# Kernel optimization log

Hardware: AMD Instinct MI355X
Metric: run time of the kernel (lower is better)

Reference implementation:

```python
import jax, jax.numpy as jnp
import numpy as np

N_NODES = 100_000
N_EDGES = 1_600_000
N_GRAPHS = 64
NUM_TYPES = 8192
EMBED = 64
HID = 128
N_STEPS = 6
N_ETYPES = 3
OUT = 1


def setup_inputs() -> dict:
    key = jax.random.key(0)
    ks = jax.random.split(key, 20)
    s = 0.05
    return {
        "type_ids": jax.random.randint(ks[0], (N_NODES,), 0, NUM_TYPES),
        "src": jax.random.randint(ks[1], (N_EDGES,), 0, N_NODES),
        "dst": jax.random.randint(ks[2], (N_EDGES,), 0, N_NODES),
        "etypes": jax.random.randint(ks[3], (N_EDGES,), 0, N_ETYPES),
        "graph_ids": jnp.sort(jax.random.randint(ks[4], (N_NODES,), 0, N_GRAPHS)),
        "embed_table": jax.random.normal(ks[5], (NUM_TYPES, EMBED)) * s,
        "W_red": jax.random.normal(ks[6], (HID, EMBED)) * s,
        "b_red": jnp.zeros((HID,)),
        "W_msg": jax.random.normal(ks[7], (N_ETYPES, HID, HID)) * s,
        "b_msg": jnp.zeros((N_ETYPES, HID)),
        "W_ih": jax.random.normal(ks[8], (3 * HID, HID)) * s,
        "b_ih": jnp.zeros((3 * HID,)),
        "W_hh": jax.random.normal(ks[9], (3 * HID, HID)) * s,
        "b_hh": jnp.zeros((3 * HID,)),
        "W_gate": jax.random.normal(ks[10], (1, 2 * HID)) * s,
        "b_gate": jnp.zeros((1,)),
        "W_out": jax.random.normal(ks[11], (OUT, 2 * HID)) * s,
        "b_out": jnp.zeros((OUT,)),
    }


def _gru_cell(x, h, W_ih, b_ih, W_hh, b_hh):
    gi = x @ W_ih.T + b_ih  # [N, 3H]
    gh = h @ W_hh.T + b_hh
    i_r, i_z, i_n = jnp.split(gi, 3, axis=-1)
    h_r, h_z, h_n = jnp.split(gh, 3, axis=-1)
    r = jax.nn.sigmoid(i_r + h_r)
    z = jax.nn.sigmoid(i_z + h_z)
    n = jnp.tanh(i_n + r * h_n)
    return (1.0 - z) * n + z * h


def reference(type_ids, src, dst, etypes, graph_ids, embed_table, W_red, b_red,
              W_msg, b_msg, W_ih, b_ih, W_hh, b_hh, W_gate, b_gate, W_out, b_out):
    ann = embed_table[type_ids]                 # [N, EMBED]
    h0 = ann @ W_red.T + b_red                  # [N, HID]
    h = h0
    edge_idx = etypes * N_NODES + src           # flat index into [K*N, H]
    for _ in range(N_STEPS):
        # per-etype linear applied at node level, then gathered per edge
        trans = jnp.einsum('nh,kdh->knd', h, W_msg) + b_msg[:, None, :]  # [K,N,H]
        msg = trans.reshape(N_ETYPES * N_NODES, HID)[edge_idx]           # [E,H]
        a = jax.ops.segment_sum(msg, dst, num_segments=N_NODES)          # [N,H]
        h = _gru_cell(a, h, W_ih, b_ih, W_hh, b_hh)
    feat = jnp.concatenate([h, h0], axis=-1)    # [N, 2H]
    # global attention pooling: segment softmax over graphs
    gate = feat @ W_gate.T + b_gate             # [N,1]
    m = jax.ops.segment_max(gate, graph_ids, num_segments=N_GRAPHS)
    e = jnp.exp(gate - m[graph_ids])
    ssum = jax.ops.segment_sum(e, graph_ids, num_segments=N_GRAPHS)
    alpha = e / ssum[graph_ids]                 # [N,1]
    readout = jax.ops.segment_sum(alpha * feat, graph_ids, num_segments=N_GRAPHS)
    return readout @ W_out.T + b_out            # [G, OUT]
```

## Files before the change

kernel.cpp:

```cpp
#include <hip/hip_runtime.h>

#define NN 100000
#define NE 1600000
#define NG 64

typedef __attribute__((ext_vector_type(8))) short bf16x8;
typedef __attribute__((ext_vector_type(4))) float f32x4;

__device__ __forceinline__ unsigned short f2bf(float f) {
  unsigned u = __float_as_uint(f);
  unsigned r = u + 0x7FFFu + ((u >> 16) & 1u);
  return (unsigned short)(r >> 16);
}
__device__ __forceinline__ float bf2f(unsigned u16) {
  return __uint_as_float(u16 << 16);
}

__device__ __forceinline__ float wave_sum(float v) {
#pragma unroll
  for (int off = 32; off; off >>= 1) v += __shfl_down(v, off, 64);
  return v;
}
__device__ __forceinline__ float wave_max(float v) {
#pragma unroll
  for (int off = 32; off; off >>= 1) v = fmaxf(v, __shfl_down(v, off, 64));
  return v;
}

__device__ __forceinline__ float sigm(float v) { return 1.f / (1.f + __expf(-v)); }

__global__ void __launch_bounds__(256)
gather_k(const unsigned* __restrict__ hbf32, const int* __restrict__ rowst,
         const int* __restrict__ payload, unsigned short* __restrict__ S) {
  const int lane = threadIdx.x & 63, wid = threadIdx.x >> 6;
  int task = blockIdx.x * 4 + wid;
  if (task >= 3 * NN) return;
  const int s = rowst[task], e = rowst[task + 1];
  float sx = 0.f, sy = 0.f;
  int i = s;
  for (; i + 4 <= e; i += 4) {
    int p0 = payload[i], p1 = payload[i + 1], p2 = payload[i + 2], p3 = payload[i + 3];
    unsigned v0 = hbf32[(size_t)p0 * 64 + lane];
    unsigned v1 = hbf32[(size_t)p1 * 64 + lane];
    unsigned v2 = hbf32[(size_t)p2 * 64 + lane];
    unsigned v3 = hbf32[(size_t)p3 * 64 + lane];
    sx += bf2f(v0 & 0xffffu) + bf2f(v1 & 0xffffu) + bf2f(v2 & 0xffffu) + bf2f(v3 & 0xffffu);
    sy += bf2f(v0 >> 16) + bf2f(v1 >> 16) + bf2f(v2 >> 16) + bf2f(v3 >> 16);
  }
  const int rem = e - i;
  if (rem == 3) {
    int p0 = payload[i], p1 = payload[i + 1], p2 = payload[i + 2];
    unsigned v0 = hbf32[(size_t)p0 * 64 + lane];
    unsigned v1 = hbf32[(size_t)p1 * 64 + lane];
    unsigned v2 = hbf32[(size_t)p2 * 64 + lane];
    sx += bf2f(v0 & 0xffffu) + bf2f(v1 & 0xffffu) + bf2f(v2 & 0xffffu);
    sy += bf2f(v0 >> 16) + bf2f(v1 >> 16) + bf2f(v2 >> 16);
  } else if (rem == 2) {
    int p0 = payload[i], p1 = payload[i + 1];
    unsigned v0 = hbf32[(size_t)p0 * 64 + lane];
    unsigned v1 = hbf32[(size_t)p1 * 64 + lane];
    sx += bf2f(v0 & 0xffffu) + bf2f(v1 & 0xffffu);
    sy += bf2f(v0 >> 16) + bf2f(v1 >> 16);
  } else if (rem == 1) {
    int p0 = payload[i];
    unsigned v0 = hbf32[(size_t)p0 * 64 + lane];
    sx += bf2f(v0 & 0xffffu);
    sy += bf2f(v0 >> 16);
  }
  const int et = task / NN;
  const int n = task - et * NN;
  unsigned pk = (unsigned)f2bf(sx) | ((unsigned)f2bf(sy) << 16);
  *(unsigned*)(S + (size_t)n * 384 + et * 128 + 2 * lane) = pk;
}

__global__ void pack_fragB(const float* __restrict__ W, unsigned short* __restrict__ WF) {
  int idx = blockIdx.x * 256 + threadIdx.x;
  if (idx >= 3 * 4 * 8 * 64) return;
  int lane = idx & 63;
  int cc = (idx >> 6) & 7;
  int ks = (idx >> 9) & 3;
  int g = idx >> 11;
  int col = cc * 16 + (lane & 15);
  int k0 = ks * 32 + (lane >> 4) * 8;
  const float* src = W + ((size_t)g * 128 + col) * 128 + k0;
  bf16x8 o;
#pragma unroll
  for (int j = 0; j < 8; ++j) o[j] = (short)f2bf(src[j]);
  *(bf16x8*)(WF + (size_t)idx * 8) = o;
}

__global__ void pack_rz(const float* __restrict__ Wih, const float* __restrict__ Whh,
                        unsigned short* __restrict__ WF) {
  int idx = blockIdx.x * 256 + threadIdx.x;
  if (idx >= 2 * 8 * 8 * 64) return;
  int lane = idx & 63;
  int cc = (idx >> 6) & 7;
  int ks = (idx >> 9) & 7;
  int g = idx >> 12;
  int col = cc * 16 + (lane & 15);
  int k0 = ks * 32 + (lane >> 4) * 8;
  int row = g * 128 + col;
  const float* src = (k0 < 128) ? (Wih + (size_t)row * 128 + k0)
                                : (Whh + (size_t)row * 128 + (k0 - 128));
  bf16x8 o;
#pragma unroll
  for (int j = 0; j < 8; ++j) o[j] = (short)f2bf(src[j]);
  *(bf16x8*)(WF + (size_t)idx * 8) = o;
}

__global__ void pack_cat384(const float* __restrict__ Wmsg, unsigned short* __restrict__ WF) {
  int idx = blockIdx.x * 256 + threadIdx.x;
  if (idx >= 12 * 8 * 64) return;
  int lane = idx & 63;
  int cc = (idx >> 6) & 7;
  int ks = idx >> 9;
  int col = cc * 16 + (lane & 15);
  int k0 = ks * 32 + (lane >> 4) * 8;
  int et = k0 >> 7, h0 = k0 & 127;
  const float* src = Wmsg + (size_t)et * 16384 + (size_t)col * 128 + h0;
  bf16x8 o;
#pragma unroll
  for (int j = 0; j < 8; ++j) o[j] = (short)f2bf(src[j]);
  *(bf16x8*)(WF + (size_t)idx * 8) = o;
}

__global__ void __launch_bounds__(256, 4)
msg_gemm6(const unsigned short* __restrict__ S, const unsigned short* __restrict__ WcatF,
          const float* __restrict__ bmsg, const int* __restrict__ rowst,
          unsigned short* __restrict__ abf) {
  __shared__ char Ss[24576];
  const int tid = threadIdx.x, lane = tid & 63, wid = tid >> 6;
  const int l15 = lane & 15, lhi = lane >> 4;
  const int bm = blockIdx.x * 32;
  const int wrow0 = (wid >> 1) * 16, wcol0 = (wid & 1) * 64;

  for (int idx = tid; idx < 1536; idx += 256) {
    int row = idx / 48, o = (idx - row * 48) * 16;
    int gr = bm + row;
    uint4 v = make_uint4(0, 0, 0, 0);
    if (gr < NN) v = *(const uint4*)((const char*)S + (size_t)gr * 768 + o);
    *(uint4*)(Ss + row * 768 + (o ^ ((row & 7) << 4))) = v;
  }
  __syncthreads();

  f32x4 acc[4];
#pragma unroll
  for (int f = 0; f < 4; ++f)
#pragma unroll
    for (int r = 0; r < 4; ++r) acc[f][r] = 0.f;

#pragma unroll
  for (int ks = 0; ks < 12; ++ks) {
    int kb = ks * 64 + lhi * 16;
    int row = wrow0 + l15;
    bf16x8 fS = *(const bf16x8*)(Ss + row * 768 + (kb ^ ((row & 7) << 4)));
#pragma unroll
    for (int nf = 0; nf < 4; ++nf) {
      bf16x8 bw = *(const bf16x8*)(WcatF +
          (((size_t)ks * 8 + (wcol0 >> 4) + nf) * 64 + lane) * 8);
      acc[nf] = __builtin_amdgcn_mfma_f32_16x16x32_bf16(fS, bw, acc[nf], 0, 0, 0);
    }
  }

#pragma unroll
  for (int r = 0; r < 4; ++r) {
    int grow = bm + wrow0 + lhi * 4 + r;
    if (grow >= NN) continue;
    float d0 = (float)(rowst[grow + 1] - rowst[grow]);
    float d1 = (float)(rowst[NN + grow + 1] - rowst[NN + grow]);
    float d2 = (float)(rowst[2 * NN + grow + 1] - rowst[2 * NN + grow]);
#pragma unroll
    for (int nf = 0; nf < 4; ++nf) {
      int col = wcol0 + nf * 16 + l15;
      float v = acc[nf][r] + d0 * bmsg[col] + d1 * bmsg[128 + col] +
                d2 * bmsg[256 + col];
      abf[(size_t)grow * 128 + col] = f2bf(v);
    }
  }
}

__global__ void __launch_bounds__(256, 4)
gru6(unsigned short* __restrict__ hbf, unsigned short* __restrict__ hlo,
     const unsigned short* __restrict__ abf, const unsigned short* __restrict__ WrzF,
     const unsigned short* __restrict__ WihF, const unsigned short* __restrict__ WhhF,
     const float* __restrict__ bih, const float* __restrict__ bhh) {
  __shared__ char cat[32 * 512];
  const int tid = threadIdx.x, lane = tid & 63, wid = tid >> 6;
  const int l15 = lane & 15, lhi = lane >> 4;
  const int bm = blockIdx.x * 32;
  const int wrow0 = (wid >> 1) * 16, wcol0 = (wid & 1) * 64;

  for (int idx = tid; idx < 1024; idx += 256) {
    int row = idx >> 5, seg = idx & 31;
    int gr = bm + row;
    uint4 v = make_uint4(0, 0, 0, 0);
    if (gr < NN) {
      if (seg < 16)
        v = *(const uint4*)((const char*)abf + (size_t)gr * 256 + seg * 16);
      else
        v = *(const uint4*)((const char*)hbf + (size_t)gr * 256 + (seg - 16) * 16);
    }
    int o = seg * 16;
    *(uint4*)(cat + row * 512 + (o ^ ((row & 7) << 4))) = v;
  }
  __syncthreads();

  f32x4 rr[4];
  {
    f32x4 acc[4];
#pragma unroll
    for (int f = 0; f < 4; ++f)
#pragma unroll
      for (int r = 0; r < 4; ++r) acc[f][r] = 0.f;
#pragma unroll
    for (int ks = 0; ks < 8; ++ks) {
      int kb = ks * 64 + lhi * 16;
      int row = wrow0 + l15;
      bf16x8 fA = *(const bf16x8*)(cat + row * 512 + (kb ^ ((row & 7) << 4)));
#pragma unroll
      for (int nf = 0; nf < 4; ++nf) {
        bf16x8 bw = *(const bf16x8*)(WrzF +
            (((size_t)ks * 8 + (wcol0 >> 4) + nf) * 64 + lane) * 8);
        acc[nf] = __builtin_amdgcn_mfma_f32_16x16x32_bf16(fA, bw, acc[nf], 0, 0, 0);
      }
    }
#pragma unroll
    for (int f = 0; f < 4; ++f) {
      int col = wcol0 + f * 16 + l15;
      float b = bih[col] + bhh[col];
#pragma unroll
      for (int r = 0; r < 4; ++r) rr[f][r] = sigm(acc[f][r] + b);
    }
  }

  f32x4 nn[4];
  {
    f32x4 acc_i[4], acc_h[4];
#pragma unroll
    for (int f = 0; f < 4; ++f)
#pragma unroll
      for (int r = 0; r < 4; ++r) { acc_i[f][r] = 0.f; acc_h[f][r] = 0.f; }
#pragma unroll
    for (int ks = 0; ks < 4; ++ks) {
      int kb = ks * 64 + lhi * 16;
      int row = wrow0 + l15;
      int sw = (row & 7) << 4;
      bf16x8 fa = *(const bf16x8*)(cat + row * 512 + (kb ^ sw));
      bf16x8 fh = *(const bf16x8*)(cat + row * 512 + ((256 + kb) ^ sw));
#pragma unroll
      for (int nf = 0; nf < 4; ++nf) {
        size_t fidx = (((size_t)(2 * 4 + ks) * 8 + (wcol0 >> 4) + nf) * 64 + lane) * 8;
        bf16x8 bi = *(const bf16x8*)(WihF + fidx);
        bf16x8 bh = *(const bf16x8*)(WhhF + fidx);
        acc_i[nf] = __builtin_amdgcn_mfma_f32_16x16x32_bf16(fa, bi, acc_i[nf], 0, 0, 0);
        acc_h[nf] = __builtin_amdgcn_mfma_f32_16x16x32_bf16(fh, bh, acc_h[nf], 0, 0, 0);
      }
    }
#pragma unroll
    for (int f = 0; f < 4; ++f) {
      int col = wcol0 + f * 16 + l15;
      float bi = bih[256 + col], bh = bhh[256 + col];
#pragma unroll
      for (int r = 0; r < 4; ++r) {
        float x = acc_i[f][r] + bi + rr[f][r] * (acc_h[f][r] + bh);
        float e = __expf(-2.f * x);
        nn[f][r] = (1.f - e) / (1.f + e);
      }
    }
  }

  {
    f32x4 acc[4];
#pragma unroll
    for (int f = 0; f < 4; ++f)
#pragma unroll
      for (int r = 0; r < 4; ++r) acc[f][r] = 0.f;
#pragma unroll
    for (int ks = 0; ks < 8; ++ks) {
      int kb = ks * 64 + lhi * 16;
      int row = wrow0 + l15;
      bf16x8 fA = *(const bf16x8*)(cat + row * 512 + (kb ^ ((row & 7) << 4)));
#pragma unroll
      for (int nf = 0; nf < 4; ++nf) {
        bf16x8 bw = *(const bf16x8*)(WrzF +
            (((size_t)(8 + ks) * 8 + (wcol0 >> 4) + nf) * 64 + lane) * 8);
        acc[nf] = __builtin_amdgcn_mfma_f32_16x16x32_bf16(fA, bw, acc[nf], 0, 0, 0);
      }
    }
#pragma unroll
    for (int r = 0; r < 4; ++r) {
      int m = wrow0 + lhi * 4 + r;
      int grow = bm + m;
      if (grow >= NN) continue;
      int sw = (m & 7) << 4;
#pragma unroll
      for (int nf = 0; nf < 4; ++nf) {
        int col = wcol0 + nf * 16 + l15;
        float zv = sigm(acc[nf][r] + bih[128 + col] + bhh[128 + col]);
        float hoh = bf2f(*(const unsigned short*)(cat + m * 512 + ((256 + 2 * col) ^ sw)));
        float hol = bf2f(hlo[(size_t)grow * 128 + col]);
        float hv = (1.f - zv) * nn[nf][r] + zv * (hoh + hol);
        unsigned short hi = f2bf(hv);
        hbf[(size_t)grow * 128 + col] = hi;
        hlo[(size_t)grow * 128 + col] = f2bf(hv - bf2f(hi));
      }
    }
  }
}

template <int KD>
__global__ void __launch_bounds__(256)
gemm_cacheB(const float* __restrict__ X, const int* __restrict__ rowidx,
            const float* __restrict__ B, int ldb, const float* __restrict__ bias,
            float* __restrict__ C, int M) {
  __shared__ float xs[KD * 64];
  constexpr int KC = KD / 4;
  const int tid = threadIdx.x;
  const int bm = blockIdx.x * 64;

  for (int idx = tid; idx < 64 * KC; idx += 256) {
    int m = idx / KC, c = idx - m * KC;
    int gm = bm + m;
    float4 v = make_float4(0.f, 0.f, 0.f, 0.f);
    if (gm < M) {
      int r = rowidx ? rowidx[gm] : gm;
      v = *(const float4*)(X + (size_t)r * KD + 4 * c);
    }
    int k0 = 4 * c;
    xs[(k0 + 0) * 64 + ((((m >> 2) ^ ((k0 + 0) & 15)) << 2) | (m & 3))] = v.x;
    xs[(k0 + 1) * 64 + ((((m >> 2) ^ ((k0 + 1) & 15)) << 2) | (m & 3))] = v.y;
    xs[(k0 + 2) * 64 + ((((m >> 2) ^ ((k0 + 2) & 15)) << 2) | (m & 3))] = v.z;
    xs[(k0 + 3) * 64 + ((((m >> 2) ^ ((k0 + 3) & 15)) << 2) | (m & 3))] = v.w;
  }
  __syncthreads();

  const int tx = tid & 15, ty = tid >> 4;
  float acc[4][8] = {};
#pragma unroll 4
  for (int k = 0; k < KD; ++k) {
    float4 a = *(float4*)(xs + k * 64 + ((ty ^ (k & 15)) << 2));
    float4 b0 = *(const float4*)(B + (size_t)k * ldb + 4 * tx);
    float4 b1 = *(const float4*)(B + (size_t)k * ldb + 64 + 4 * tx);
    float av[4] = {a.x, a.y, a.z, a.w};
    float bv[8] = {b0.x, b0.y, b0.z, b0.w, b1.x, b1.y, b1.z, b1.w};
#pragma unroll
    for (int i = 0; i < 4; ++i)
#pragma unroll
      for (int j = 0; j < 8; ++j) acc[i][j] += av[i] * bv[j];
  }

#pragma unroll
  for (int i = 0; i < 4; ++i) {
    int gm = bm + 4 * ty + i;
    if (gm >= M) continue;
    float4 o0, o1;
    o0.x = acc[i][0] + bias[4 * tx + 0];
    o0.y = acc[i][1] + bias[4 * tx + 1];
    o0.z = acc[i][2] + bias[4 * tx + 2];
    o0.w = acc[i][3] + bias[4 * tx + 3];
    o1.x = acc[i][4] + bias[64 + 4 * tx + 0];
    o1.y = acc[i][5] + bias[64 + 4 * tx + 1];
    o1.z = acc[i][6] + bias[64 + 4 * tx + 2];
    o1.w = acc[i][7] + bias[64 + 4 * tx + 3];
    *(float4*)(C + (size_t)gm * 128 + 4 * tx) = o0;
    *(float4*)(C + (size_t)gm * 128 + 64 + 4 * tx) = o1;
  }
}

__global__ void count3_k(const int* __restrict__ dst, const int* __restrict__ et,
                         int* __restrict__ deg3) {
  int e = blockIdx.x * 256 + threadIdx.x;
  if (e < NE) atomicAdd(&deg3[et[e] * NN + dst[e]], 1);
}
__global__ void scan1(const int* __restrict__ deg, int* __restrict__ rowst,
                      int* __restrict__ csum, int L) {
  __shared__ int s[256];
  int base = blockIdx.x * 1024;
  int tid = threadIdx.x;
  int v[4], pre[4];
  int run = 0;
#pragma unroll
  for (int j = 0; j < 4; ++j) {
    int idx = base + tid * 4 + j;
    v[j] = (idx < L) ? deg[idx] : 0;
    pre[j] = run;
    run += v[j];
  }
  s[tid] = run;
  __syncthreads();
  for (int off = 1; off < 256; off <<= 1) {
    int t = (tid >= off) ? s[tid - off] : 0;
    __syncthreads();
    s[tid] += t;
    __syncthreads();
  }
  int excl = (tid == 0) ? 0 : s[tid - 1];
#pragma unroll
  for (int j = 0; j < 4; ++j) {
    int idx = base + tid * 4 + j;
    if (idx < L) rowst[idx] = excl + pre[j];
  }
  if (tid == 255) csum[blockIdx.x] = s[255];
}
__global__ void scan2(int* csum, int nch) {
  if (threadIdx.x == 0 && blockIdx.x == 0) {
    int run = 0;
    for (int i = 0; i < nch; ++i) { int t = csum[i]; csum[i] = run; run += t; }
  }
}
__global__ void scan3(int* rowst, const int* __restrict__ csum, int L) {
  int idx = blockIdx.x * 256 + threadIdx.x;
  if (idx < L) rowst[idx] += csum[idx >> 10];
}
__global__ void set_last(int* rowst) { rowst[3 * NN] = NE; }
__global__ void fill3_k(const int* __restrict__ src, const int* __restrict__ dst,
                        const int* __restrict__ et, const int* __restrict__ rowst3,
                        int* __restrict__ cursor3, int* __restrict__ payload) {
  int e = blockIdx.x * 256 + threadIdx.x;
  if (e >= NE) return;
  int b3 = et[e] * NN + dst[e];
  int pos = rowst3[b3] + atomicAdd(&cursor3[b3], 1);
  payload[pos] = src[e];
}

__global__ void transpose_w(const float* __restrict__ W, float* __restrict__ WT,
                            int J, int Kd) {
  int idx = blockIdx.x * 256 + threadIdx.x;
  if (idx >= J * Kd) return;
  int j = idx / Kd, k = idx - j * Kd;
  WT[(size_t)k * J + j] = W[idx];
}

__global__ void conv_hilo(const float* __restrict__ s, unsigned short* __restrict__ dhi,
                          unsigned short* __restrict__ dlo, int n4) {
  int i = blockIdx.x * 256 + threadIdx.x;
  if (i >= n4) return;
  float4 v = *(const float4*)(s + 4 * (size_t)i);
  unsigned short h0 = f2bf(v.x), h1 = f2bf(v.y), h2 = f2bf(v.z), h3 = f2bf(v.w);
  uint2 hp, lp;
  hp.x = (unsigned)h0 | ((unsigned)h1 << 16);
  hp.y = (unsigned)h2 | ((unsigned)h3 << 16);
  lp.x = (unsigned)f2bf(v.x - bf2f(h0)) | ((unsigned)f2bf(v.y - bf2f(h1)) << 16);
  lp.y = (unsigned)f2bf(v.z - bf2f(h2)) | ((unsigned)f2bf(v.w - bf2f(h3)) << 16);
  *(uint2*)(dhi + 4 * (size_t)i) = hp;
  *(uint2*)(dlo + 4 * (size_t)i) = lp;
}

__global__ void __launch_bounds__(256)
nodeval_k(const unsigned* __restrict__ hhi, const unsigned* __restrict__ hlow,
          const float* __restrict__ h0, const float* __restrict__ Wg,
          const float* __restrict__ bg, const float* __restrict__ Wout,
          float* __restrict__ gate, float* __restrict__ cbuf) {
  int wid = threadIdx.x >> 6, lane = threadIdx.x & 63;
  int n = blockIdx.x * 4 + wid;
  if (n >= NN) return;
  unsigned hi = hhi[(size_t)n * 64 + lane];
  unsigned lo = hlow[(size_t)n * 64 + lane];
  float hx = bf2f(hi & 0xffffu) + bf2f(lo & 0xffffu);
  float hy = bf2f(hi >> 16) + bf2f(lo >> 16);
  float2 h0v = *(const float2*)(h0 + (size_t)n * 128 + 2 * lane);
  float pg = hx * Wg[2 * lane] + hy * Wg[2 * lane + 1] +
             h0v.x * Wg[128 + 2 * lane] + h0v.y * Wg[128 + 2 * lane + 1];
  float pc = hx * Wout[2 * lane] + hy * Wout[2 * lane + 1] +
             h0v.x * Wout[128 + 2 * lane] + h0v.y * Wout[128 + 2 * lane + 1];
  pg = wave_sum(pg);
  pc = wave_sum(pc);
  if (lane == 0) {
    gate[n] = pg + bg[0];
    cbuf[n] = pc;
  }
}

__global__ void bounds_k(const int* __restrict__ gid, int* __restrict__ bound) {
  int g = threadIdx.x;
  if (g > NG) return;
  int lo = 0, hi = NN;
  while (lo < hi) {
    int mid = (lo + hi) >> 1;
    if (gid[mid] < g) lo = mid + 1; else hi = mid;
  }
  bound[g] = lo;
}

__global__ void __launch_bounds__(256)
finalize_k(const float* __restrict__ gate, const float* __restrict__ cbuf,
           const int* __restrict__ bound, const float* __restrict__ bout,
           float* __restrict__ out) {
  int g = blockIdx.x;
  int s = bound[g], e = bound[g + 1];
  __shared__ float sred[4], sred2[4];
  __shared__ float sm;
  int tid = threadIdx.x, wid = tid >> 6, lane = tid & 63;
  if (s >= e) { if (tid == 0) out[g] = bout[0]; return; }

  float mx = -3.4e38f;
  for (int i = s + tid; i < e; i += 256) mx = fmaxf(mx, gate[i]);
  mx = wave_max(mx);
  if (lane == 0) sred[wid] = mx;
  __syncthreads();
  if (tid == 0) sm = fmaxf(fmaxf(sred[0], sred[1]), fmaxf(sred[2], sred[3]));
  __syncthreads();
  float m = sm;

  float ss = 0.f, cs = 0.f;
  for (int i = s + tid; i < e; i += 256) {
    float w = __expf(gate[i] - m);
    ss += w;
    cs += w * cbuf[i];
  }
  ss = wave_sum(ss);
  cs = wave_sum(cs);
  if (lane == 0) { sred[wid] = ss; sred2[wid] = cs; }
  __syncthreads();
  if (tid == 0) {
    float S = sred[0] + sred[1] + sred[2] + sred[3];
    float C = sred2[0] + sred2[1] + sred2[2] + sred2[3];
    out[g] = C / S + bout[0];
  }
}

extern "C" void kernel_launch(void* const* d_in, const int* in_sizes, int n_in,
                              void* d_out, int out_size, void* d_ws, size_t ws_size,
                              hipStream_t stream) {
  (void)in_sizes; (void)n_in; (void)out_size; (void)ws_size;
  const int* type_ids = (const int*)d_in[0];
  const int* src      = (const int*)d_in[1];
  const int* dst      = (const int*)d_in[2];
  const int* etypes   = (const int*)d_in[3];
  const int* gid      = (const int*)d_in[4];
  const float* embed  = (const float*)d_in[5];
  const float* W_red  = (const float*)d_in[6];
  const float* b_red  = (const float*)d_in[7];
  const float* W_msg  = (const float*)d_in[8];
  const float* b_msg  = (const float*)d_in[9];
  const float* W_ih   = (const float*)d_in[10];
  const float* b_ih   = (const float*)d_in[11];
  const float* W_hh   = (const float*)d_in[12];
  const float* b_hh   = (const float*)d_in[13];
  const float* W_gate = (const float*)d_in[14];
  const float* b_gate = (const float*)d_in[15];
  const float* W_out  = (const float*)d_in[16];
  const float* b_out  = (const float*)d_in[17];

  char* p = (char*)d_ws;
  auto take = [&](size_t nb) { char* r = p; p += (nb + 255) & ~(size_t)255; return r; };
  float* h0b           = (float*)take((size_t)NN * 128 * sizeof(float));
  unsigned short* hbf  = (unsigned short*)take((size_t)NN * 128 * 2);
  unsigned short* hlo  = (unsigned short*)take((size_t)NN * 128 * 2);
  unsigned short* abf  = (unsigned short*)take((size_t)NN * 128 * 2);
  unsigned short* Sbuf = (unsigned short*)take((size_t)NN * 384 * 2);
  unsigned short* WcatF = (unsigned short*)take(12 * 8 * 64 * 8 * 2);
  unsigned short* WrzF  = (unsigned short*)take(2 * 8 * 8 * 64 * 8 * 2);
  unsigned short* WihF  = (unsigned short*)take(49152 * 2);
  unsigned short* WhhF  = (unsigned short*)take(49152 * 2);
  float* WredT         = (float*)take(64 * 128 * sizeof(float));
  float* gateb         = (float*)take((size_t)NN * sizeof(float));
  float* cbuf          = (float*)take((size_t)NN * sizeof(float));
  int* deg3    = (int*)take((size_t)2 * 3 * NN * sizeof(int));
  int* cursor3 = deg3 + 3 * NN;
  int* rowst3x = (int*)take(((size_t)3 * NN + 1) * sizeof(int));
  int* payload = (int*)take((size_t)NE * sizeof(int));
  int* csum    = (int*)take(2048);
  int* bound   = (int*)take(512);

  transpose_w<<<(128 * 64 + 255) / 256, 256, 0, stream>>>(W_red, WredT, 128, 64);
  pack_cat384<<<(12 * 8 * 64 + 255) / 256, 256, 0, stream>>>(W_msg, WcatF);
  pack_rz<<<(2 * 8 * 8 * 64 + 255) / 256, 256, 0, stream>>>(W_ih, W_hh, WrzF);
  pack_fragB<<<24, 256, 0, stream>>>(W_ih, WihF);
  pack_fragB<<<24, 256, 0, stream>>>(W_hh, WhhF);

  const int L3 = 3 * NN;
  hipMemsetAsync(deg3, 0, (size_t)2 * L3 * sizeof(int), stream);
  count3_k<<<(NE + 255) / 256, 256, 0, stream>>>(dst, etypes, deg3);
  int nch = (L3 + 1023) / 1024;
  scan1<<<nch, 256, 0, stream>>>(deg3, rowst3x, csum, L3);
  scan2<<<1, 64, 0, stream>>>(csum, nch);
  scan3<<<(L3 + 255) / 256, 256, 0, stream>>>(rowst3x, csum, L3);
  set_last<<<1, 1, 0, stream>>>(rowst3x);
  fill3_k<<<(NE + 255) / 256, 256, 0, stream>>>(src, dst, etypes, rowst3x, cursor3, payload);

  gemm_cacheB<64><<<(NN + 63) / 64, 256, 0, stream>>>(
      embed, type_ids, WredT, 128, b_red, h0b, NN);
  conv_hilo<<<((NN * 128 / 4) + 255) / 256, 256, 0, stream>>>(h0b, hbf, hlo, NN * 128 / 4);

  const int nblk32 = (NN + 31) / 32;
  const int ngb = (3 * NN + 3) / 4;
  for (int s6 = 0; s6 < 6; ++s6) {
    gather_k<<<ngb, 256, 0, stream>>>((const unsigned*)hbf, rowst3x, payload, Sbuf);
    msg_gemm6<<<nblk32, 256, 0, stream>>>(Sbuf, WcatF, b_msg, rowst3x, abf);
    gru6<<<nblk32, 256, 0, stream>>>(hbf, hlo, abf, WrzF, WihF, WhhF, b_ih, b_hh);
  }

  nodeval_k<<<(NN + 3) / 4, 256, 0, stream>>>((const unsigned*)hbf, (const unsigned*)hlo,
                                              h0b, W_gate, b_gate, W_out, gateb, cbuf);
  bounds_k<<<1, 128, 0, stream>>>(gid, bound);
  finalize_k<<<NG, 256, 0, stream>>>(gateb, cbuf, bound, b_out, (float*)d_out);
}
```

Baseline: 1.472 ms.

## Fuse message GEMM and GRU into one kernel, keeping aggregated messages in LDS

After: 2.307 ms. +56.7%, slower.

```diff
diff --git a/kernel.cpp b/kernel.cpp
--- a/kernel.cpp
+++ b/kernel.cpp
@@ -124,11 +124,16 @@
   *(bf16x8*)(WF + (size_t)idx * 8) = o;
 }
 
-__global__ void __launch_bounds__(256, 4)
-msg_gemm6(const unsigned short* __restrict__ S, const unsigned short* __restrict__ WcatF,
-          const float* __restrict__ bmsg, const int* __restrict__ rowst,
-          unsigned short* __restrict__ abf) {
-  __shared__ char Ss[24576];
+__global__ void __launch_bounds__(256, 6)
+msggru32(unsigned short* __restrict__ hbf, unsigned short* __restrict__ hlo,
+         const unsigned short* __restrict__ S, const unsigned short* __restrict__ WcatF,
+         const float* __restrict__ bmsg, const int* __restrict__ rowst,
+         const unsigned short* __restrict__ WrzF, const unsigned short* __restrict__ WihF,
+         const unsigned short* __restrict__ WhhF, const float* __restrict__ bih,
+         const float* __restrict__ bhh) {
+  __shared__ char lds[24576];
+  char* Ss = lds;
+  char* cat = lds;
   const int tid = threadIdx.x, lane = tid & 63, wid = tid >> 6;
   const int l15 = lane & 15, lhi = lane >> 4;
   const int bm = blockIdx.x * 32;
@@ -143,65 +148,53 @@
   }
   __syncthreads();
 
-  f32x4 acc[4];
-#pragma unroll
-  for (int f = 0; f < 4; ++f)
-#pragma unroll
-    for (int r = 0; r < 4; ++r) acc[f][r] = 0.f;
-
-#pragma unroll
-  for (int ks = 0; ks < 12; ++ks) {
-    int kb = ks * 64 + lhi * 16;
-    int row = wrow0 + l15;
-    bf16x8 fS = *(const bf16x8*)(Ss + row * 768 + (kb ^ ((row & 7) << 4)));
-#pragma unroll
-    for (int nf = 0; nf < 4; ++nf) {
-      bf16x8 bw = *(const bf16x8*)(WcatF +
-          (((size_t)ks * 8 + (wcol0 >> 4) + nf) * 64 + lane) * 8);
-      acc[nf] = __builtin_amdgcn_mfma_f32_16x16x32_bf16(fS, bw, acc[nf], 0, 0, 0);
-    }
-  }
-
-#pragma unroll
-  for (int r = 0; r < 4; ++r) {
-    int grow = bm + wrow0 + lhi * 4 + r;
-    if (grow >= NN) continue;
-    float d0 = (float)(rowst[grow + 1] - rowst[grow]);
-    float d1 = (float)(rowst[NN + grow + 1] - rowst[NN + grow]);
-    float d2 = (float)(rowst[2 * NN + grow + 1] - rowst[2 * NN + grow]);
-#pragma unroll
-    for (int nf = 0; nf < 4; ++nf) {
-      int col = wcol0 + nf * 16 + l15;
-      float v = acc[nf][r] + d0 * bmsg[col] + d1 * bmsg[128 + col] +
-                d2 * bmsg[256 + col];
-      abf[(size_t)grow * 128 + col] = f2bf(v);
-    }
-  }
-}
-
-__global__ void __launch_bounds__(256, 4)
-gru6(unsigned short* __restrict__ hbf, unsigned short* __restrict__ hlo,
-     const unsigned short* __restrict__ abf, const unsigned short* __restrict__ WrzF,
-     const unsigned short* __restrict__ WihF, const unsigned short* __restrict__ WhhF,
-     const float* __restrict__ bih, const float* __restrict__ bhh) {
-  __shared__ char cat[32 * 512];
-  const int tid = threadIdx.x, lane = tid & 63, wid = tid >> 6;
-  const int l15 = lane & 15, lhi = lane >> 4;
-  const int bm = blockIdx.x * 32;
-  const int wrow0 = (wid >> 1) * 16, wcol0 = (wid & 1) * 64;
-
-  for (int idx = tid; idx < 1024; idx += 256) {
-    int row = idx >> 5, seg = idx & 31;
+  {
+    f32x4 acc[4];
+#pragma unroll
+    for (int f = 0; f < 4; ++f)
+#pragma unroll
+      for (int r = 0; r < 4; ++r) acc[f][r] = 0.f;
+
+#pragma unroll
+    for (int ks = 0; ks < 12; ++ks) {
+      int kb = ks * 64 + lhi * 16;
+      int row = wrow0 + l15;
+      bf16x8 fS = *(const bf16x8*)(Ss + row * 768 + (kb ^ ((row & 7) << 4)));
+#pragma unroll
+      for (int nf = 0; nf < 4; ++nf) {
+        bf16x8 bw = *(const bf16x8*)(WcatF +
+            (((size_t)ks * 8 + (wcol0 >> 4) + nf) * 64 + lane) * 8);
+        acc[nf] = __builtin_amdgcn_mfma_f32_16x16x32_bf16(fS, bw, acc[nf], 0, 0, 0);
+      }
+    }
+    __syncthreads();
+
+#pragma unroll
+    for (int r = 0; r < 4; ++r) {
+      int m = wrow0 + lhi * 4 + r;
+      int grow = bm + m;
+      float d0 = 0.f, d1 = 0.f, d2 = 0.f;
+      if (grow < NN) {
+        d0 = (float)(rowst[grow + 1] - rowst[grow]);
+        d1 = (float)(rowst[NN + grow + 1] - rowst[NN + grow]);
+        d2 = (float)(rowst[2 * NN + grow + 1] - rowst[2 * NN + grow]);
+      }
+      int sw = (m & 7) << 4;
+#pragma unroll
+      for (int nf = 0; nf < 4; ++nf) {
+        int col = wcol0 + nf * 16 + l15;
+        float v = acc[nf][r] + d0 * bmsg[col] + d1 * bmsg[128 + col] +
+                  d2 * bmsg[256 + col];
+        *(unsigned short*)(cat + m * 512 + ((2 * col) ^ sw)) = f2bf(v);
+      }
+    }
+  }
+  for (int idx = tid; idx < 512; idx += 256) {
+    int row = idx >> 4, seg = idx & 15;
     int gr = bm + row;
-    uint4 v = make_uint4(0, 0, 0, 0);
-    if (gr < NN) {
-      if (seg < 16)
-        v = *(const uint4*)((const char*)abf + (size_t)gr * 256 + seg * 16);
-      else
-        v = *(const uint4*)((const char*)hbf + (size_t)gr * 256 + (seg - 16) * 16);
-    }
-    int o = seg * 16;
-    *(uint4*)(cat + row * 512 + (o ^ ((row & 7) << 4))) = v;
+    uint4 vh = make_uint4(0, 0, 0, 0);
+    if (gr < NN) vh = *(const uint4*)((const char*)hbf + (size_t)gr * 256 + seg * 16);
+    *(uint4*)(cat + row * 512 + ((256 + seg * 16) ^ ((row & 7) << 4))) = vh;
   }
   __syncthreads();
 
@@ -547,7 +540,6 @@
   float* h0b           = (float*)take((size_t)NN * 128 * sizeof(float));
   unsigned short* hbf  = (unsigned short*)take((size_t)NN * 128 * 2);
   unsigned short* hlo  = (unsigned short*)take((size_t)NN * 128 * 2);
-  unsigned short* abf  = (unsigned short*)take((size_t)NN * 128 * 2);
   unsigned short* Sbuf = (unsigned short*)take((size_t)NN * 384 * 2);
   unsigned short* WcatF = (unsigned short*)take(12 * 8 * 64 * 8 * 2);
   unsigned short* WrzF  = (unsigned short*)take(2 * 8 * 8 * 64 * 8 * 2);
@@ -587,8 +579,8 @@
   const int ngb = (3 * NN + 3) / 4;
   for (int s6 = 0; s6 < 6; ++s6) {
     gather_k<<<ngb, 256, 0, stream>>>((const unsigned*)hbf, rowst3x, payload, Sbuf);
-    msg_gemm6<<<nblk32, 256, 0, stream>>>(Sbuf, WcatF, b_msg, rowst3x, abf);
-    gru6<<<nblk32, 256, 0, stream>>>(hbf, hlo, abf, WrzF, WihF, WhhF, b_ih, b_hh);
+    msggru32<<<nblk32, 256, 0, stream>>>(hbf, hlo, Sbuf, WcatF, b_msg, rowst3x,
+                                         WrzF, WihF, WhhF, b_ih, b_hh);
   }
 
   nodeval_k<<<(NN + 3) / 4, 256, 0, stream>>>((const unsigned*)hbf, (const unsigned*)hlo,
```
